# Optimization experiments

Measured on AMD Instinct MI355X. Metric: run time of the kernel, lower is better.

## Reference

```python
import jax, jax.numpy as jnp
import numpy as np

B, IN, H, OUT = 4096, 1024, 1024, 1024


def setup_inputs() -> dict:
    key = jax.random.key(0)
    ks = jax.random.split(key, 16)
    s_in = 1.0 / np.sqrt(IN)
    s_h = 1.0 / np.sqrt(H)
    d = {}
    d['input_vec'] = jax.random.normal(ks[0], (B, IN), jnp.float32)
    d['hidden_vec'] = jax.random.normal(ks[1], (B, H), jnp.float32)
    d['cell_vec'] = jax.random.normal(ks[2], (B, H), jnp.float32)
    names = ['f', 'i', 'o', 'g']
    for j, n in enumerate(names):
        d['Wx_' + n] = jax.random.uniform(ks[3 + 3 * j], (H, IN), jnp.float32, -s_in, s_in)
        d['bx_' + n] = jax.random.uniform(ks[4 + 3 * j], (H,), jnp.float32, -s_in, s_in)
        d['Wh_' + n] = jax.random.uniform(ks[5 + 3 * j], (H, H), jnp.float32, -s_h, s_h)
    d['W_out'] = jax.random.uniform(ks[15], (OUT, H), jnp.float32, -s_h, s_h)
    d['b_out'] = jax.random.uniform(jax.random.fold_in(key, 99), (OUT,), jnp.float32, -s_h, s_h)
    return d


def reference(input_vec, hidden_vec, cell_vec,
              Wx_f, bx_f, Wh_f,
              Wx_i, bx_i, Wh_i,
              Wx_o, bx_o, Wh_o,
              Wx_g, bx_g, Wh_g,
              W_out, b_out):
    # Fuse the 8 small linears into two GEMMs: [B,IN]x[IN,4H] and [B,H]x[H,4H].
    Wx = jnp.concatenate([Wx_f, Wx_i, Wx_o, Wx_g], axis=0)   # [4H, IN]
    Wh = jnp.concatenate([Wh_f, Wh_i, Wh_o, Wh_g], axis=0)   # [4H, H]
    b = jnp.concatenate([bx_f, bx_i, bx_o, bx_g], axis=0)    # [4H]
    gates = input_vec @ Wx.T + hidden_vec @ Wh.T + b          # [B, 4H]
    f, i, o, g = jnp.split(gates, 4, axis=1)
    f = jax.nn.sigmoid(f)
    i = jax.nn.sigmoid(i)
    o = jax.nn.sigmoid(o)
    g = jnp.tanh(g)
    new_cell = f * cell_vec + i * g
    new_hidden = o * jnp.tanh(new_cell)
    output_vec = new_hidden @ W_out.T + b_out
    return (new_hidden, new_cell, output_vec)
```

## Files before the change

kernel.cpp:

```cpp
#include <hip/hip_runtime.h>
#include <hip/hip_bf16.h>
#include <stdint.h>

#define B_   4096
#define IN_  1024
#define H_   1024
#define OUT_ 1024

typedef __attribute__((ext_vector_type(8)))  short short8;
typedef __attribute__((ext_vector_type(16))) float floatx16;

__device__ static inline void gload_lds16(const void* g, void* l) {
    __builtin_amdgcn_global_load_lds(
        (const __attribute__((address_space(1))) unsigned int*)g,
        (__attribute__((address_space(3))) unsigned int*)l,
        16, 0, 0);
}

__device__ static inline float sigmoidf_(float x) { return 1.0f / (1.0f + __expf(-x)); }
__device__ static inline float tanhf_(float x)    { return 1.0f - 2.0f / (1.0f + __expf(2.0f * x)); }

struct Ptrs8 { const float* p[8]; };

__global__ void cvt_all_kernel(const float* __restrict__ x, const float* __restrict__ h,
                               Ptrs8 ptrs, const float* __restrict__ wout,
                               __hip_bfloat16* __restrict__ xh,
                               __hip_bfloat16* __restrict__ Wc,
                               __hip_bfloat16* __restrict__ Wob) {
    int blk = blockIdx.x;
    const float* src;
    __hip_bfloat16* dst;
    if (blk < 8192) {
        int idx = blk * 256 + threadIdx.x;
        int b  = idx >> 9;
        int c4 = (idx & 511) * 4;
        src = (c4 < IN_) ? (x + (size_t)b * IN_ + c4)
                         : (h + (size_t)b * H_ + (c4 - IN_));
        dst = xh + (size_t)b * 2048 + c4;
    } else if (blk < 16384) {
        int idx = (blk - 8192) * 256 + threadIdx.x;
        int n  = idx >> 9;
        int c4 = (idx & 511) * 4;
        int gate = (n >> 5) & 3;
        int hh   = ((n >> 7) << 5) + (n & 31);
        src = (c4 < 1024) ? (ptrs.p[2 * gate]     + (size_t)hh * 1024 + c4)
                          : (ptrs.p[2 * gate + 1] + (size_t)hh * 1024 + (c4 - 1024));
        dst = Wc + (size_t)n * 2048 + c4;
    } else {
        int idx = (blk - 16384) * 256 + threadIdx.x;
        src = wout + (size_t)idx * 4;
        dst = Wob + (size_t)idx * 4;
    }
    float4 v = *(const float4*)src;
    dst[0] = __float2bfloat16(v.x);
    dst[1] = __float2bfloat16(v.y);
    dst[2] = __float2bfloat16(v.z);
    dst[3] = __float2bfloat16(v.w);
}

__global__ __launch_bounds__(256) void gemm_gate_fused(
    const __hip_bfloat16* __restrict__ A,
    const __hip_bfloat16* __restrict__ Bm,
    const float* __restrict__ cell,
    const float* __restrict__ bxf, const float* __restrict__ bxi,
    const float* __restrict__ bxo, const float* __restrict__ bxg,
    float* __restrict__ new_hidden, float* __restrict__ new_cell,
    __hip_bfloat16* __restrict__ hb)
{
    constexpr int BK = 64;
    constexpr int K  = 2048;
    constexpr int N  = 4096;

    __shared__ __hip_bfloat16 ldsA[128 * BK];
    __shared__ __hip_bfloat16 ldsB[128 * BK];

    const int tid  = threadIdx.x;
    const int lane = tid & 63;
    const int wv   = tid >> 6;

    const int bid    = blockIdx.x;
    const int xcd    = bid & 7;
    const int loc    = bid >> 3;
    const int n_tile = xcd * 4 + (loc & 3);
    const int m_tile = loc >> 2;
    const int m0 = m_tile * 128;
    const int n0 = n_tile * 128;

    const int srow   = tid >> 3;
    const int schunk = tid & 7;
    const int scg    = schunk ^ (srow & 7);
    const __hip_bfloat16* Ag = A  + (size_t)(m0 + srow) * K + scg * 8;
    const __hip_bfloat16* Bg = Bm + (size_t)(n0 + srow) * K + scg * 8;
    char* lA = (char*)ldsA + wv * 1024;
    char* lB = (char*)ldsB + wv * 1024;

    const int wrow  = wv * 32;
    const int fr    = lane & 31;
    const int khalf = lane >> 5;

    floatx16 acc[4] = {};

    for (int k0 = 0; k0 < K; k0 += BK) {
        #pragma unroll
        for (int s = 0; s < 4; ++s)
            gload_lds16(Ag + (size_t)(s * 32) * K + k0, lA + s * 4096);
        #pragma unroll
        for (int s = 0; s < 4; ++s)
            gload_lds16(Bg + (size_t)(s * 32) * K + k0, lB + s * 4096);
        __syncthreads();

        #pragma unroll
        for (int kk = 0; kk < 4; ++kk) {
            const int cg = kk * 2 + khalf;
            const int ra = wrow + fr;
            short8 af = *(const short8*)((const char*)ldsA + ra * 128 + ((cg ^ (ra & 7)) * 16));
            short8 bf[4];
            #pragma unroll
            for (int j = 0; j < 4; ++j) {
                const int r = j * 32 + fr;
                bf[j] = *(const short8*)((const char*)ldsB + r * 128 + ((cg ^ (r & 7)) * 16));
            }
            #pragma unroll
            for (int j = 0; j < 4; ++j)
                acc[j] = __builtin_amdgcn_mfma_f32_32x32x16_bf16(af, bf[j], acc[j], 0, 0, 0);
        }
        __syncthreads();
    }

    const int h  = (n0 >> 2) + fr;
    const float bfb = bxf[h];
    const float bib = bxi[h];
    const float bob = bxo[h];
    const float bgb = bxg[h];
    const int row_base = m0 + wrow + 4 * khalf;

    #pragma unroll
    for (int reg = 0; reg < 16; ++reg) {
        const int row = row_base + (reg & 3) + 8 * (reg >> 2);
        const size_t off = (size_t)row * H_ + h;
        const float f = sigmoidf_(acc[0][reg] + bfb);
        const float i = sigmoidf_(acc[1][reg] + bib);
        const float o = sigmoidf_(acc[2][reg] + bob);
        const float g = tanhf_(acc[3][reg] + bgb);
        const float c = f * cell[off] + i * g;
        const float nh = o * tanhf_(c);
        new_cell[off]   = c;
        new_hidden[off] = nh;
        hb[off] = __float2bfloat16(nh);
    }
}

__global__ __launch_bounds__(256) void gemm_out(
    const __hip_bfloat16* __restrict__ A,
    const __hip_bfloat16* __restrict__ Bm,
    float* __restrict__ C,
    const float* __restrict__ bias)
{
    constexpr int BK = 64;
    constexpr int K  = 1024;
    constexpr int N  = 1024;

    __shared__ __hip_bfloat16 ldsA[128 * BK];
    __shared__ __hip_bfloat16 ldsB[64 * BK];

    const int tid  = threadIdx.x;
    const int lane = tid & 63;
    const int wv   = tid >> 6;

    const int bid    = blockIdx.x;
    const int xcd    = bid & 7;
    const int loc    = bid >> 3;
    const int n_tile = xcd * 2 + (loc & 1);
    const int m_tile = loc >> 1;
    const int m0 = m_tile * 128;
    const int n0 = n_tile * 64;

    const int srow   = tid >> 3;
    const int schunk = tid & 7;
    const int scg    = schunk ^ (srow & 7);
    const __hip_bfloat16* Ag = A  + (size_t)(m0 + srow) * K + scg * 8;
    const __hip_bfloat16* Bg = Bm + (size_t)(n0 + srow) * K + scg * 8;
    char* lA = (char*)ldsA + wv * 1024;
    char* lB = (char*)ldsB + wv * 1024;

    const int wrow  = wv * 32;
    const int fr    = lane & 31;
    const int khalf = lane >> 5;

    floatx16 acc[2] = {};

    for (int k0 = 0; k0 < K; k0 += BK) {
        #pragma unroll
        for (int s = 0; s < 4; ++s)
            gload_lds16(Ag + (size_t)(s * 32) * K + k0, lA + s * 4096);
        #pragma unroll
        for (int s = 0; s < 2; ++s)
            gload_lds16(Bg + (size_t)(s * 32) * K + k0, lB + s * 4096);
        __syncthreads();

        #pragma unroll
        for (int kk = 0; kk < 4; ++kk) {
            const int cg = kk * 2 + khalf;
            const int ra = wrow + fr;
            short8 af = *(const short8*)((const char*)ldsA + ra * 128 + ((cg ^ (ra & 7)) * 16));
            short8 bf[2];
            #pragma unroll
            for (int j = 0; j < 2; ++j) {
                const int r = j * 32 + fr;
                bf[j] = *(const short8*)((const char*)ldsB + r * 128 + ((cg ^ (r & 7)) * 16));
            }
            #pragma unroll
            for (int j = 0; j < 2; ++j)
                acc[j] = __builtin_amdgcn_mfma_f32_32x32x16_bf16(af, bf[j], acc[j], 0, 0, 0);
        }
        __syncthreads();
    }

    #pragma unroll
    for (int j = 0; j < 2; ++j) {
        const int col = n0 + j * 32 + fr;
        const float bb = bias[col];
        #pragma unroll
        for (int reg = 0; reg < 16; ++reg) {
            const int row = m0 + wrow + 4 * khalf + (reg & 3) + 8 * (reg >> 2);
            C[(size_t)row * N + col] = acc[j][reg] + bb;
        }
    }
}

extern "C" void kernel_launch(void* const* d_in, const int* in_sizes, int n_in,
                              void* d_out, int out_size, void* d_ws, size_t ws_size,
                              hipStream_t stream) {
    const float* input_vec  = (const float*)d_in[0];
    const float* hidden_vec = (const float*)d_in[1];
    const float* cell_vec   = (const float*)d_in[2];
    const float* Wx_f = (const float*)d_in[3];
    const float* bx_f = (const float*)d_in[4];
    const float* Wh_f = (const float*)d_in[5];
    const float* Wx_i = (const float*)d_in[6];
    const float* bx_i = (const float*)d_in[7];
    const float* Wh_i = (const float*)d_in[8];
    const float* Wx_o = (const float*)d_in[9];
    const float* bx_o = (const float*)d_in[10];
    const float* Wh_o = (const float*)d_in[11];
    const float* Wx_g = (const float*)d_in[12];
    const float* bx_g = (const float*)d_in[13];
    const float* Wh_g = (const float*)d_in[14];
    const float* W_out = (const float*)d_in[15];
    const float* b_out = (const float*)d_in[16];

    char* ws = (char*)d_ws;
    __hip_bfloat16* xh  = (__hip_bfloat16*)(ws);
    __hip_bfloat16* Wc  = (__hip_bfloat16*)(ws + (16ull << 20));
    __hip_bfloat16* Wob = (__hip_bfloat16*)(ws + (32ull << 20));
    __hip_bfloat16* hb  = (__hip_bfloat16*)(ws + (34ull << 20));

    float* new_hidden = (float*)d_out;
    float* new_cell   = new_hidden + (size_t)B_ * H_;
    float* out_vec    = new_cell + (size_t)B_ * H_;

    Ptrs8 p;
    p.p[0] = Wx_f; p.p[1] = Wh_f; p.p[2] = Wx_i; p.p[3] = Wh_i;
    p.p[4] = Wx_o; p.p[5] = Wh_o; p.p[6] = Wx_g; p.p[7] = Wh_g;
    cvt_all_kernel<<<17408, 256, 0, stream>>>(input_vec, hidden_vec, p, W_out, xh, Wc, Wob);

    gemm_gate_fused<<<1024, 256, 0, stream>>>(
        xh, Wc, cell_vec, bx_f, bx_i, bx_o, bx_g, new_hidden, new_cell, hb);

    gemm_out<<<512, 256, 0, stream>>>(hb, Wob, out_vec, b_out);
}
```

Measured before the change: 249.0 us.

## Double M tile to 256 rows per block in both GEMMs

Both GEMM kernels now compute 256-row M tiles instead of 128, so each wave holds two A fragments and reuses every loaded B fragment across them. This halves the grid size and cuts redundant B (weight) loads and LDS traffic per MFMA. In exchange it doubles accumulator registers and LDS per block and leaves fewer blocks to spread over the CUs. A launch-bounds hint of 2 blocks per CU is added to keep occupancy up.

```diff
diff --git a/kernel.cpp b/kernel.cpp
--- a/kernel.cpp
+++ b/kernel.cpp
@@ -58,7 +58,7 @@
     dst[3] = __float2bfloat16(v.w);
 }
 
-__global__ __launch_bounds__(256) void gemm_gate_fused(
+__global__ __launch_bounds__(256, 2) void gemm_gate_fused(
     const __hip_bfloat16* __restrict__ A,
     const __hip_bfloat16* __restrict__ Bm,
     const float* __restrict__ cell,
@@ -69,9 +69,8 @@
 {
     constexpr int BK = 64;
     constexpr int K  = 2048;
-    constexpr int N  = 4096;
-
-    __shared__ __hip_bfloat16 ldsA[128 * BK];
+
+    __shared__ __hip_bfloat16 ldsA[256 * BK];
     __shared__ __hip_bfloat16 ldsB[128 * BK];
 
     const int tid  = threadIdx.x;
@@ -83,7 +82,7 @@
     const int loc    = bid >> 3;
     const int n_tile = xcd * 4 + (loc & 3);
     const int m_tile = loc >> 2;
-    const int m0 = m_tile * 128;
+    const int m0 = m_tile * 256;
     const int n0 = n_tile * 128;
 
     const int srow   = tid >> 3;
@@ -94,15 +93,15 @@
     char* lA = (char*)ldsA + wv * 1024;
     char* lB = (char*)ldsB + wv * 1024;
 
-    const int wrow  = wv * 32;
+    const int wrow  = wv * 64;
     const int fr    = lane & 31;
     const int khalf = lane >> 5;
 
-    floatx16 acc[4] = {};
+    floatx16 acc[2][4] = {};
 
     for (int k0 = 0; k0 < K; k0 += BK) {
         #pragma unroll
-        for (int s = 0; s < 4; ++s)
+        for (int s = 0; s < 8; ++s)
             gload_lds16(Ag + (size_t)(s * 32) * K + k0, lA + s * 4096);
         #pragma unroll
         for (int s = 0; s < 4; ++s)
@@ -112,17 +111,22 @@
         #pragma unroll
         for (int kk = 0; kk < 4; ++kk) {
             const int cg = kk * 2 + khalf;
-            const int ra = wrow + fr;
-            short8 af = *(const short8*)((const char*)ldsA + ra * 128 + ((cg ^ (ra & 7)) * 16));
-            short8 bf[4];
+            short8 af[2], bf[4];
+            #pragma unroll
+            for (int i = 0; i < 2; ++i) {
+                const int r = wrow + i * 32 + fr;
+                af[i] = *(const short8*)((const char*)ldsA + r * 128 + ((cg ^ (r & 7)) * 16));
+            }
             #pragma unroll
             for (int j = 0; j < 4; ++j) {
                 const int r = j * 32 + fr;
                 bf[j] = *(const short8*)((const char*)ldsB + r * 128 + ((cg ^ (r & 7)) * 16));
             }
             #pragma unroll
-            for (int j = 0; j < 4; ++j)
-                acc[j] = __builtin_amdgcn_mfma_f32_32x32x16_bf16(af, bf[j], acc[j], 0, 0, 0);
+            for (int i = 0; i < 2; ++i)
+                #pragma unroll
+                for (int j = 0; j < 4; ++j)
+                    acc[i][j] = __builtin_amdgcn_mfma_f32_32x32x16_bf16(af[i], bf[j], acc[i][j], 0, 0, 0);
         }
         __syncthreads();
     }
@@ -132,25 +136,28 @@
     const float bib = bxi[h];
     const float bob = bxo[h];
     const float bgb = bxg[h];
-    const int row_base = m0 + wrow + 4 * khalf;
 
     #pragma unroll
-    for (int reg = 0; reg < 16; ++reg) {
-        const int row = row_base + (reg & 3) + 8 * (reg >> 2);
-        const size_t off = (size_t)row * H_ + h;
-        const float f = sigmoidf_(acc[0][reg] + bfb);
-        const float i = sigmoidf_(acc[1][reg] + bib);
-        const float o = sigmoidf_(acc[2][reg] + bob);
-        const float g = tanhf_(acc[3][reg] + bgb);
-        const float c = f * cell[off] + i * g;
-        const float nh = o * tanhf_(c);
-        new_cell[off]   = c;
-        new_hidden[off] = nh;
-        hb[off] = __float2bfloat16(nh);
-    }
-}
-
-__global__ __launch_bounds__(256) void gemm_out(
+    for (int i = 0; i < 2; ++i) {
+        const int row_base = m0 + wrow + i * 32 + 4 * khalf;
+        #pragma unroll
+        for (int reg = 0; reg < 16; ++reg) {
+            const int row = row_base + (reg & 3) + 8 * (reg >> 2);
+            const size_t off = (size_t)row * H_ + h;
+            const float f = sigmoidf_(acc[i][0][reg] + bfb);
+            const float ii = sigmoidf_(acc[i][1][reg] + bib);
+            const float o = sigmoidf_(acc[i][2][reg] + bob);
+            const float g = tanhf_(acc[i][3][reg] + bgb);
+            const float c = f * cell[off] + ii * g;
+            const float nh = o * tanhf_(c);
+            new_cell[off]   = c;
+            new_hidden[off] = nh;
+            hb[off] = __float2bfloat16(nh);
+        }
+    }
+}
+
+__global__ __launch_bounds__(256, 2) void gemm_out(
     const __hip_bfloat16* __restrict__ A,
     const __hip_bfloat16* __restrict__ Bm,
     float* __restrict__ C,
@@ -160,7 +167,7 @@
     constexpr int K  = 1024;
     constexpr int N  = 1024;
 
-    __shared__ __hip_bfloat16 ldsA[128 * BK];
+    __shared__ __hip_bfloat16 ldsA[256 * BK];
     __shared__ __hip_bfloat16 ldsB[64 * BK];
 
     const int tid  = threadIdx.x;
@@ -172,7 +179,7 @@
     const int loc    = bid >> 3;
     const int n_tile = xcd * 2 + (loc & 1);
     const int m_tile = loc >> 1;
-    const int m0 = m_tile * 128;
+    const int m0 = m_tile * 256;
     const int n0 = n_tile * 64;
 
     const int srow   = tid >> 3;
@@ -183,15 +190,15 @@
     char* lA = (char*)ldsA + wv * 1024;
     char* lB = (char*)ldsB + wv * 1024;
 
-    const int wrow  = wv * 32;
+    const int wrow  = wv * 64;
     const int fr    = lane & 31;
     const int khalf = lane >> 5;
 
-    floatx16 acc[2] = {};
+    floatx16 acc[2][2] = {};
 
     for (int k0 = 0; k0 < K; k0 += BK) {
         #pragma unroll
-        for (int s = 0; s < 4; ++s)
+        for (int s = 0; s < 8; ++s)
             gload_lds16(Ag + (size_t)(s * 32) * K + k0, lA + s * 4096);
         #pragma unroll
         for (int s = 0; s < 2; ++s)
@@ -201,17 +208,22 @@
         #pragma unroll
         for (int kk = 0; kk < 4; ++kk) {
             const int cg = kk * 2 + khalf;
-            const int ra = wrow + fr;
-            short8 af = *(const short8*)((const char*)ldsA + ra * 128 + ((cg ^ (ra & 7)) * 16));
-            short8 bf[2];
+            short8 af[2], bf[2];
+            #pragma unroll
+            for (int i = 0; i < 2; ++i) {
+                const int r = wrow + i * 32 + fr;
+                af[i] = *(const short8*)((const char*)ldsA + r * 128 + ((cg ^ (r & 7)) * 16));
+            }
             #pragma unroll
             for (int j = 0; j < 2; ++j) {
                 const int r = j * 32 + fr;
                 bf[j] = *(const short8*)((const char*)ldsB + r * 128 + ((cg ^ (r & 7)) * 16));
             }
             #pragma unroll
-            for (int j = 0; j < 2; ++j)
-                acc[j] = __builtin_amdgcn_mfma_f32_32x32x16_bf16(af, bf[j], acc[j], 0, 0, 0);
+            for (int i = 0; i < 2; ++i)
+                #pragma unroll
+                for (int j = 0; j < 2; ++j)
+                    acc[i][j] = __builtin_amdgcn_mfma_f32_32x32x16_bf16(af[i], bf[j], acc[i][j], 0, 0, 0);
         }
         __syncthreads();
     }
@@ -221,9 +233,12 @@
         const int col = n0 + j * 32 + fr;
         const float bb = bias[col];
         #pragma unroll
-        for (int reg = 0; reg < 16; ++reg) {
-            const int row = m0 + wrow + 4 * khalf + (reg & 3) + 8 * (reg >> 2);
-            C[(size_t)row * N + col] = acc[j][reg] + bb;
+        for (int i = 0; i < 2; ++i) {
+            #pragma unroll
+            for (int reg = 0; reg < 16; ++reg) {
+                const int row = m0 + wrow + i * 32 + 4 * khalf + (reg & 3) + 8 * (reg >> 2);
+                C[(size_t)row * N + col] = acc[i][j][reg] + bb;
+            }
         }
     }
 }
@@ -264,8 +279,8 @@
     p.p[4] = Wx_o; p.p[5] = Wh_o; p.p[6] = Wx_g; p.p[7] = Wh_g;
     cvt_all_kernel<<<17408, 256, 0, stream>>>(input_vec, hidden_vec, p, W_out, xh, Wc, Wob);
 
-    gemm_gate_fused<<<1024, 256, 0, stream>>>(
+    gemm_gate_fused<<<512, 256, 0, stream>>>(
         xh, Wc, cell_vec, bx_f, bx_i, bx_o, bx_g, new_hidden, new_cell, hb);
 
-    gemm_out<<<512, 256, 0, stream>>>(hb, Wob, out_vec, b_out);
-}
+    gemm_out<<<256, 256, 0, stream>>>(hb, Wob, out_vec, b_out);
+}
```

New measurement: 251.5 us. About the same (+1.0%).

## Use 2x2 wave tiling in gate GEMM with 16-wide gate interleave and shuffle epilogue

Applied to the files above, without the earlier changes.

Changes the gate GEMM's per-wave tile from 32x128 (one A fragment, four B fragments) to 64x64 (two A, two B fragments), which cuts LDS fragment reads per MFMA. To keep each wave holding all four gates for its hidden units, the weight interleave becomes 16 rows per gate instead of 32. The epilogue then uses lane shuffles to gather f/i/o/g, and each lane handles half the rows. It also adds occupancy hints to launch_bounds on both GEMMs, at the cost of shuffle overhead and predicated work in the epilogue.

```diff
diff --git a/kernel.cpp b/kernel.cpp
--- a/kernel.cpp
+++ b/kernel.cpp
@@ -41,8 +41,8 @@
         int idx = (blk - 8192) * 256 + threadIdx.x;
         int n  = idx >> 9;
         int c4 = (idx & 511) * 4;
-        int gate = (n >> 5) & 3;
-        int hh   = ((n >> 7) << 5) + (n & 31);
+        int gate = (n >> 4) & 3;
+        int hh   = ((n >> 6) << 4) + (n & 15);
         src = (c4 < 1024) ? (ptrs.p[2 * gate]     + (size_t)hh * 1024 + c4)
                           : (ptrs.p[2 * gate + 1] + (size_t)hh * 1024 + (c4 - 1024));
         dst = Wc + (size_t)n * 2048 + c4;
@@ -58,7 +58,7 @@
     dst[3] = __float2bfloat16(v.w);
 }
 
-__global__ __launch_bounds__(256) void gemm_gate_fused(
+__global__ __launch_bounds__(256, 4) void gemm_gate_fused(
     const __hip_bfloat16* __restrict__ A,
     const __hip_bfloat16* __restrict__ Bm,
     const float* __restrict__ cell,
@@ -69,7 +69,6 @@
 {
     constexpr int BK = 64;
     constexpr int K  = 2048;
-    constexpr int N  = 4096;
 
     __shared__ __hip_bfloat16 ldsA[128 * BK];
     __shared__ __hip_bfloat16 ldsB[128 * BK];
@@ -94,11 +93,12 @@
     char* lA = (char*)ldsA + wv * 1024;
     char* lB = (char*)ldsB + wv * 1024;
 
-    const int wrow  = wv * 32;
+    const int wrow  = (wv >> 1) * 64;
+    const int wcol  = (wv & 1) * 64;
     const int fr    = lane & 31;
     const int khalf = lane >> 5;
 
-    floatx16 acc[4] = {};
+    floatx16 acc[2][2] = {};
 
     for (int k0 = 0; k0 < K; k0 += BK) {
         #pragma unroll
@@ -112,45 +112,64 @@
         #pragma unroll
         for (int kk = 0; kk < 4; ++kk) {
             const int cg = kk * 2 + khalf;
-            const int ra = wrow + fr;
-            short8 af = *(const short8*)((const char*)ldsA + ra * 128 + ((cg ^ (ra & 7)) * 16));
-            short8 bf[4];
-            #pragma unroll
-            for (int j = 0; j < 4; ++j) {
-                const int r = j * 32 + fr;
+            short8 af[2], bf[2];
+            #pragma unroll
+            for (int i = 0; i < 2; ++i) {
+                const int r = wrow + i * 32 + fr;
+                af[i] = *(const short8*)((const char*)ldsA + r * 128 + ((cg ^ (r & 7)) * 16));
+            }
+            #pragma unroll
+            for (int j = 0; j < 2; ++j) {
+                const int r = wcol + j * 32 + fr;
                 bf[j] = *(const short8*)((const char*)ldsB + r * 128 + ((cg ^ (r & 7)) * 16));
             }
             #pragma unroll
-            for (int j = 0; j < 4; ++j)
-                acc[j] = __builtin_amdgcn_mfma_f32_32x32x16_bf16(af, bf[j], acc[j], 0, 0, 0);
-        }
-        __syncthreads();
-    }
-
-    const int h  = (n0 >> 2) + fr;
+            for (int i = 0; i < 2; ++i)
+                #pragma unroll
+                for (int j = 0; j < 2; ++j)
+                    acc[i][j] = __builtin_amdgcn_mfma_f32_32x32x16_bf16(af[i], bf[j], acc[i][j], 0, 0, 0);
+        }
+        __syncthreads();
+    }
+
+    const int h = ((n0 + wcol) >> 6) * 16 + (fr & 15);
     const float bfb = bxf[h];
     const float bib = bxi[h];
     const float bob = bxo[h];
     const float bgb = bxg[h];
-    const int row_base = m0 + wrow + 4 * khalf;
+    const bool low = (fr < 16);
 
     #pragma unroll
-    for (int reg = 0; reg < 16; ++reg) {
-        const int row = row_base + (reg & 3) + 8 * (reg >> 2);
-        const size_t off = (size_t)row * H_ + h;
-        const float f = sigmoidf_(acc[0][reg] + bfb);
-        const float i = sigmoidf_(acc[1][reg] + bib);
-        const float o = sigmoidf_(acc[2][reg] + bob);
-        const float g = tanhf_(acc[3][reg] + bgb);
-        const float c = f * cell[off] + i * g;
-        const float nh = o * tanhf_(c);
-        new_cell[off]   = c;
-        new_hidden[off] = nh;
-        hb[off] = __float2bfloat16(nh);
-    }
-}
-
-__global__ __launch_bounds__(256) void gemm_out(
+    for (int i = 0; i < 2; ++i) {
+        const int row_base = m0 + wrow + i * 32 + 4 * khalf;
+        #pragma unroll
+        for (int reg = 0; reg < 16; ++reg) {
+            const float v0 = acc[i][0][reg];
+            const float v1 = acc[i][1][reg];
+            const float o0 = __shfl_xor(v0, 16);
+            const float o1 = __shfl_xor(v1, 16);
+            const float fpre = low ? v0 : o0;
+            const float ipre = low ? o0 : v0;
+            const float opre = low ? v1 : o1;
+            const float gpre = low ? o1 : v1;
+            if (low == (reg < 8)) {
+                const int row = row_base + (reg & 3) + 8 * (reg >> 2);
+                const size_t off = (size_t)row * H_ + h;
+                const float f  = sigmoidf_(fpre + bfb);
+                const float ii = sigmoidf_(ipre + bib);
+                const float o  = sigmoidf_(opre + bob);
+                const float g  = tanhf_(gpre + bgb);
+                const float c  = f * cell[off] + ii * g;
+                const float nh = o * tanhf_(c);
+                new_cell[off]   = c;
+                new_hidden[off] = nh;
+                hb[off] = __float2bfloat16(nh);
+            }
+        }
+    }
+}
+
+__global__ __launch_bounds__(256, 2) void gemm_out(
     const __hip_bfloat16* __restrict__ A,
     const __hip_bfloat16* __restrict__ Bm,
     float* __restrict__ C,
```

After: 266.9 us. 1.07x slower.
